# Kernel optimization log

Measured on AMD Instinct MI355X. Metric: run time of the kernel, lower is better.

Reference implementation:

```python
import jax, jax.numpy as jnp
import numpy as np

N_NODES = 50000
N_EDGES = 800000
F_IN = 128          # num_node_features == conv_size
L = 4               # num_conv_layers
LIN = 256
OUT = 10
N_GRAPHS = 64


def setup_inputs() -> dict:
    key = jax.random.key(0)
    ks = jax.random.split(key, 8)
    x = jax.random.normal(ks[0], (N_NODES, F_IN), dtype=jnp.float32)
    edge_index = jax.random.randint(ks[1], (2, N_EDGES), 0, N_NODES, dtype=jnp.int64)
    batch = jnp.sort(jax.random.randint(ks[2], (N_NODES,), 0, N_GRAPHS, dtype=jnp.int64))
    pos = jax.random.normal(ks[3], (N_NODES, 3), dtype=jnp.float32)
    # learned params: 4 GCN layers (all [F_IN,F_IN] since in==out==128), cat-JK head
    Ws = jax.random.normal(ks[4], (L, F_IN, F_IN), dtype=jnp.float32) * 0.05
    bs = jnp.zeros((L, F_IN), dtype=jnp.float32)
    Wlin = jax.random.normal(ks[5], (L * F_IN, LIN), dtype=jnp.float32) * 0.05
    blin = jnp.zeros((LIN,), dtype=jnp.float32)
    Wout = jax.random.normal(ks[6], (LIN, OUT), dtype=jnp.float32) * 0.05
    bout = jnp.zeros((OUT,), dtype=jnp.float32)
    return {"x": x, "edge_index": edge_index, "batch": batch, "pos": pos,
            "Ws": Ws, "bs": bs, "Wlin": Wlin, "blin": blin,
            "Wout": Wout, "bout": bout}


def reference(x, edge_index, batch, pos, Ws, bs, Wlin, blin, Wout, bout):
    N = x.shape[0]
    # GCN normalization with added self-loops (PyG gcn_norm, edge_weight=1)
    loop = jnp.arange(N, dtype=edge_index.dtype)
    src = jnp.concatenate([edge_index[0], loop])
    dst = jnp.concatenate([edge_index[1], loop])
    deg = jax.ops.segment_sum(jnp.ones_like(dst, dtype=x.dtype), dst, num_segments=N)
    dinv = jax.lax.rsqrt(deg)  # deg >= 1 due to self-loops
    norm = (dinv[src] * dinv[dst])[:, None]  # [E+N, 1]

    h = x
    xs = []
    for l in range(L):
        t = h @ Ws[l]                                    # [N, F]
        agg = jax.ops.segment_sum(t[src] * norm, dst, num_segments=N)
        h = jax.nn.relu(agg + bs[l])                     # dropout is identity in eval
        xs.append(h)
    hcat = jnp.concatenate(xs, axis=-1)                  # JK 'cat' -> [N, L*F]
    g = jax.ops.segment_max(hcat, batch, num_segments=N_GRAPHS)  # global_max_pool
    return jax.nn.relu(g @ Wlin + blin) @ Wout + bout    # [N_GRAPHS, OUT]
```

## Files before the change

kernel.cpp:

```cpp
#include <hip/hip_runtime.h>
#include <stdint.h>

#define NN    50000
#define NE    800000
#define FD    128
#define NLAY  4
#define NLIN  256
#define NOUTF 10
#define NGR   64
#define NBKT  196
#define MAXB  8192
#define GEMMB 782
#define POOLB 512

typedef _Float16 half8  __attribute__((ext_vector_type(8)));
typedef _Float16 half4  __attribute__((ext_vector_type(4)));
typedef _Float16 half2t __attribute__((ext_vector_type(2)));
typedef float    f32x4  __attribute__((ext_vector_type(4)));

__device__ __forceinline__ int ld_idx(const void* p, int flag, long i){
    return flag ? (int)((const long long*)p)[i] : ((const int*)p)[i];
}

__global__ __launch_bounds__(256) void pre_k(const unsigned* __restrict__ eidx_u,
                                             const float* __restrict__ Ws,
                                             _Float16* __restrict__ WT,
                                             int* __restrict__ zbase, int zn, int zb,
                                             int* __restrict__ sent,
                                             int* __restrict__ flag){
    __shared__ int any;
    const int b = blockIdx.x, tid = threadIdx.x;
    if (b < 256){
        int idx = b*256 + tid;
        int l = idx >> 14;
        int r = idx & 16383;
        int c = r >> 7, k = r & 127;
        WT[idx] = (_Float16)Ws[(l<<14) + (k<<7) + c];
    } else if (b < 256 + zb){
        int i = (b-256)*256 + tid;
        if (i < zn) zbase[i] = 0;
    } else if (b == 256 + zb){
        if (tid < FD/2) sent[tid] = 0;
    } else {
        if (tid == 0) any = 0;
        __syncthreads();
        if (eidx_u[2*tid + 1] != 0u) atomicOr(&any, 1);
        __syncthreads();
        if (tid == 0) *flag = (any == 0) ? 1 : 0;
    }
}

__global__ __launch_bounds__(1024) void binB_k(const void* __restrict__ eidx,
                                               const int* __restrict__ flag,
                                               int* __restrict__ bktCur,
                                               unsigned* __restrict__ binned){
    __shared__ int hist[NBKT];
    __shared__ int resv[NBKT];
    __shared__ int cur[NBKT];
    const int tid = threadIdx.x;
    const int f = *flag;
    if (tid < NBKT){ hist[tid] = 0; cur[tid] = 0; }
    __syncthreads();

    int bkt[4]; unsigned pk[4];
    #pragma unroll
    for (int u = 0; u < 4; ++u){
        long e = (long)blockIdx.x*4096 + u*1024 + tid;
        if (e < NE){
            int s = ld_idx(eidx, f, e);
            int d = ld_idx(eidx, f, (long)NE + e);
            bkt[u] = d >> 8;
            pk[u]  = ((unsigned)(d & 255) << 16) | (unsigned)s;
            atomicAdd(&hist[bkt[u]], 1);
        } else bkt[u] = -1;
    }
    __syncthreads();
    if (tid < NBKT && hist[tid] > 0)
        resv[tid] = atomicAdd(&bktCur[tid], hist[tid]);
    __syncthreads();
    #pragma unroll
    for (int u = 0; u < 4; ++u){
        if (bkt[u] >= 0){
            int p = resv[bkt[u]] + atomicAdd(&cur[bkt[u]], 1);
            if ((unsigned)p < MAXB) binned[(long)bkt[u]*MAXB + p] = pk[u];
        }
    }
}

__global__ __launch_bounds__(256) void passC_k(const int* __restrict__ bktCur,
                                               const unsigned* __restrict__ binned,
                                               int* __restrict__ rp, int* __restrict__ re,
                                               float* __restrict__ dinv,
                                               unsigned short* __restrict__ cn,
                                               const void* __restrict__ batv,
                                               const int* __restrict__ flag,
                                               int* __restrict__ gstart){
    __shared__ unsigned staged[MAXB];
    __shared__ int cnt[256];
    __shared__ int sc[256];
    __shared__ int cur[256];
    const int tid = threadIdx.x;
    if (blockIdx.x >= NBKT){
        int i = (blockIdx.x - NBKT)*256 + tid;
        if (i >= NN) return;
        int f = *flag;
        int b = ld_idx(batv, f, i);
        if (i == 0){
            for (int g = 0; g <= b; ++g) gstart[g] = 0;
        } else {
            int p = ld_idx(batv, f, i-1);
            for (int g = p+1; g <= b; ++g) gstart[g] = i;
        }
        if (i == NN-1){
            for (int g = b+1; g <= NGR; ++g) gstart[g] = NN;
        }
        return;
    }
    const int b = blockIdx.x;
    int n = bktCur[b]; if (n > MAXB) n = MAXB;
    const long base = (long)b*MAXB;

    cnt[tid] = 0;
    __syncthreads();
    for (int i = tid; i < n; i += 256){
        unsigned rec = binned[base + i];
        staged[i] = rec;
        atomicAdd(&cnt[rec >> 16], 1);
    }
    __syncthreads();
    int c  = cnt[tid];
    int pc = (c + 15) & ~15;
    sc[tid] = pc;
    __syncthreads();
    for (int off = 1; off < 256; off <<= 1){
        int t = (tid >= off) ? sc[tid - off] : 0;
        __syncthreads();
        if (tid >= off) sc[tid] += t;
        __syncthreads();
    }
    int lo = sc[tid] - pc;
    int v = b*256 + tid;
    if (v < NN){
        rp[v]   = (int)base + lo;
        re[v]   = (int)base + lo + pc;
        dinv[v] = rsqrtf((float)(c + 1));
    }
    cur[tid] = lo;
    __syncthreads();
    for (int i = tid; i < n; i += 256){
        unsigned rec = staged[i];
        int j = rec >> 16;
        int p = atomicAdd(&cur[j], 1);
        cn[base + p] = (unsigned short)(rec & 0xFFFFu);
    }
    __syncthreads();
    for (int i = c; i < pc; ++i)
        cn[base + lo + i] = (unsigned short)NN;
}

template<bool F32IN, bool POOL>
__global__ __launch_bounds__(256) void gemm_k(const void* __restrict__ Av,
                                              const _Float16* __restrict__ WT,
                                              const float* __restrict__ dinv,
                                              _Float16* __restrict__ T,
                                              const _Float16* __restrict__ h,
                                              const int* __restrict__ gstart,
                                              unsigned* __restrict__ gbuf, int lpool){
    const int tid  = threadIdx.x;
    if (POOL && blockIdx.x >= GEMMB){
        __shared__ float red[4][FD];
        int pid = blockIdx.x - GEMMB;
        int g = pid >> 3, part = pid & 7;
        int lane = tid & 63, w = tid >> 6;
        int s0 = gstart[g], s1 = gstart[g+1];
        int len = s1 - s0;
        int chunk = (len + 7) >> 3;
        int a = s0 + part*chunk;
        int b = min(a + chunk, s1);
        int sub = (b - a + 3) >> 2;
        int aa = a + w*sub;
        int bb = min(aa + sub, b);
        const half2t* h2 = reinterpret_cast<const half2t*>(h);
        float m0 = 0.f, m1 = 0.f;
        for (int i = aa; i < bb; ++i){
            half2t x = h2[(long)i*64 + lane];
            m0 = fmaxf(m0, (float)x[0]);
            m1 = fmaxf(m1, (float)x[1]);
        }
        red[w][2*lane]   = m0;
        red[w][2*lane+1] = m1;
        __syncthreads();
        if (w == 0){
            float r0 = fmaxf(fmaxf(red[0][2*lane],   red[1][2*lane]),
                             fmaxf(red[2][2*lane],   red[3][2*lane]));
            float r1 = fmaxf(fmaxf(red[0][2*lane+1], red[1][2*lane+1]),
                             fmaxf(red[2][2*lane+1], red[3][2*lane+1]));
            atomicMax(&gbuf[g*(NLAY*FD) + lpool*FD + 2*lane    ], __float_as_uint(r0));
            atomicMax(&gbuf[g*(NLAY*FD) + lpool*FD + 2*lane + 1], __float_as_uint(r1));
        }
        return;
    }

    const int lane = tid & 63;
    const int wid  = tid >> 6;
    const int wr   = (wid >> 1) * 32;
    const int wc   = (wid & 1) * 64;
    const long r0  = (long)blockIdx.x * 64 + wr;
    const int lr   = lane & 15;
    const int lk   = (lane >> 4) * 8;

    half8 wf[4][4];
    #pragma unroll
    for (int n = 0; n < 4; ++n)
        #pragma unroll
        for (int kk = 0; kk < 4; ++kk)
            wf[n][kk] = *reinterpret_cast<const half8*>(WT + (wc + n*16 + lr)*FD + kk*32 + lk);

    f32x4 acc[2][4];
    #pragma unroll
    for (int m = 0; m < 2; ++m)
        #pragma unroll
        for (int n = 0; n < 4; ++n)
            acc[m][n] = (f32x4){0.f,0.f,0.f,0.f};

    #pragma unroll
    for (int kk = 0; kk < 4; ++kk){
        half8 af[2];
        #pragma unroll
        for (int m = 0; m < 2; ++m){
            long row = r0 + m*16 + lr;
            if (row < NN){
                if constexpr (F32IN){
                    const float* A = (const float*)Av;
                    float4 u0 = *reinterpret_cast<const float4*>(A + row*FD + kk*32 + lk);
                    float4 u1 = *reinterpret_cast<const float4*>(A + row*FD + kk*32 + lk + 4);
                    half8 a;
                    a[0]=(_Float16)u0.x; a[1]=(_Float16)u0.y; a[2]=(_Float16)u0.z; a[3]=(_Float16)u0.w;
                    a[4]=(_Float16)u1.x; a[5]=(_Float16)u1.y; a[6]=(_Float16)u1.z; a[7]=(_Float16)u1.w;
                    af[m] = a;
                } else {
                    const _Float16* A = (const _Float16*)Av;
                    af[m] = *reinterpret_cast<const half8*>(A + row*FD + kk*32 + lk);
                }
            } else af[m] = (half8)(_Float16)0;
        }
        #pragma unroll
        for (int m = 0; m < 2; ++m)
            #pragma unroll
            for (int n = 0; n < 4; ++n)
                acc[m][n] = __builtin_amdgcn_mfma_f32_16x16x32_f16(wf[n][kk], af[m], acc[m][n], 0, 0, 0);
    }

    #pragma unroll
    for (int m = 0; m < 2; ++m){
        long row = r0 + m*16 + lr;
        if (row >= NN) continue;
        float di = dinv[row];
        #pragma unroll
        for (int n = 0; n < 4; ++n){
            half4 o;
            o[0] = (_Float16)(acc[m][n][0] * di);
            o[1] = (_Float16)(acc[m][n][1] * di);
            o[2] = (_Float16)(acc[m][n][2] * di);
            o[3] = (_Float16)(acc[m][n][3] * di);
            *reinterpret_cast<half4*>(T + row*FD + wc + n*16 + (lane>>4)*4) = o;
        }
    }
}

__global__ __launch_bounds__(256) void agg_k(const _Float16* __restrict__ t,
                                             const int* __restrict__ rp,
                                             const int* __restrict__ re,
                                             const unsigned short* __restrict__ cn,
                                             const float* __restrict__ dinv,
                                             const float* __restrict__ bias,
                                             _Float16* __restrict__ h){
    const int lane = threadIdx.x & 63;
    const int wid  = threadIdx.x >> 6;
    const int r    = lane & 15;
    const int qb   = lane & 48;
    const int v    = blockIdx.x*16 + wid*4 + (lane >> 4);
    const half8* t8 = reinterpret_cast<const half8*>(t);

    float acc[8];
    #pragma unroll
    for (int i = 0; i < 8; ++i) acc[i] = 0.f;

    half8 sv = t8[(size_t)v*16 + r];

    const int e0 = rp[v], e1 = re[v];
    for (int base = e0; base < e1; base += 16){
        int ce = (int)cn[base + r];
        #pragma unroll
        for (int j = 0; j < 16; ++j){
            int s = __shfl(ce, qb + j);
            half8 g = t8[(size_t)s*16 + r];
            #pragma unroll
            for (int i = 0; i < 8; ++i) acc[i] += (float)g[i];
        }
    }

    float di = dinv[v];
    float4 b0 = reinterpret_cast<const float4*>(bias)[2*r];
    float4 b1 = reinterpret_cast<const float4*>(bias)[2*r+1];
    float bb[8] = {b0.x,b0.y,b0.z,b0.w,b1.x,b1.y,b1.z,b1.w};
    half8 o;
    #pragma unroll
    for (int i = 0; i < 8; ++i)
        o[i] = (_Float16)fmaxf(fmaf(acc[i] + (float)sv[i], di, bb[i]), 0.f);
    reinterpret_cast<half8*>(h)[(size_t)v*16 + r] = o;
}

__global__ __launch_bounds__(256) void pool_k(const _Float16* __restrict__ h,
                                              const int* __restrict__ gstart,
                                              unsigned* __restrict__ gbuf, int l){
    __shared__ float red[4][FD];
    int g = blockIdx.x, part = blockIdx.y;
    int tid = threadIdx.x, lane = tid & 63, w = tid >> 6;
    int s0 = gstart[g], s1 = gstart[g+1];
    int len = s1 - s0;
    int chunk = (len + 7) >> 3;
    int a = s0 + part*chunk;
    int b = min(a + chunk, s1);
    int sub = (b - a + 3) >> 2;
    int aa = a + w*sub;
    int bb = min(aa + sub, b);
    const half2t* h2 = reinterpret_cast<const half2t*>(h);
    float m0 = 0.f, m1 = 0.f;
    for (int i = aa; i < bb; ++i){
        half2t x = h2[(long)i*64 + lane];
        m0 = fmaxf(m0, (float)x[0]);
        m1 = fmaxf(m1, (float)x[1]);
    }
    red[w][2*lane]   = m0;
    red[w][2*lane+1] = m1;
    __syncthreads();
    if (w == 0){
        float r0 = fmaxf(fmaxf(red[0][2*lane],   red[1][2*lane]),
                         fmaxf(red[2][2*lane],   red[3][2*lane]));
        float r1 = fmaxf(fmaxf(red[0][2*lane+1], red[1][2*lane+1]),
                         fmaxf(red[2][2*lane+1], red[3][2*lane+1]));
        atomicMax(&gbuf[g*(NLAY*FD) + l*FD + 2*lane    ], __float_as_uint(r0));
        atomicMax(&gbuf[g*(NLAY*FD) + l*FD + 2*lane + 1], __float_as_uint(r1));
    }
}

__global__ __launch_bounds__(1024) void head_k(const unsigned* __restrict__ gbuf,
                                               const float* __restrict__ Wlin,
                                               const float* __restrict__ blin,
                                               const float* __restrict__ Wout,
                                               const float* __restrict__ bout,
                                               float* __restrict__ out){
    __shared__ float gs[NLAY*FD];
    __shared__ float ps[4][NLIN];
    __shared__ float us[NLIN];
    int g = blockIdx.x, tid = threadIdx.x;
    if (tid < NLAY*FD) gs[tid] = __uint_as_float(gbuf[g*(NLAY*FD) + tid]);
    __syncthreads();
    int c = tid & 255;
    int q = tid >> 8;
    float a = 0.f;
    #pragma unroll 8
    for (int k = q*128; k < q*128 + 128; ++k)
        a = fmaf(gs[k], Wlin[k*NLIN + c], a);
    ps[q][c] = a;
    __syncthreads();
    if (tid < NLIN){
        float u = ps[0][tid] + ps[1][tid] + ps[2][tid] + ps[3][tid] + blin[tid];
        us[tid] = fmaxf(u, 0.f);
    }
    __syncthreads();
    if (tid < NOUTF){
        float o = bout[tid];
        #pragma unroll 8
        for (int k = 0; k < NLIN; ++k) o = fmaf(us[k], Wout[k*NOUTF + tid], o);
        out[g*NOUTF + tid] = o;
    }
}

extern "C" void kernel_launch(void* const* d_in, const int* in_sizes, int n_in,
                              void* d_out, int out_size, void* d_ws, size_t ws_size,
                              hipStream_t stream){
    const float* x    = (const float*)d_in[0];
    const void*  eidx = d_in[1];
    const void*  batv = d_in[2];
    const float* Wsp  = (const float*)d_in[4];
    const float* bsp  = (const float*)d_in[5];
    const float* Wlin = (const float*)d_in[6];
    const float* blin = (const float*)d_in[7];
    const float* Wout = (const float*)d_in[8];
    const float* bout = (const float*)d_in[9];
    float* out = (float*)d_out;

    uintptr_t cur = (uintptr_t)d_ws;
    auto alloc = [&](size_t bytes)->void*{
        cur = (cur + 255) & ~(uintptr_t)255;
        void* p = (void*)cur;
        cur += bytes;
        return p;
    };
    _Float16* t    = (_Float16*)alloc((size_t)(NN+1)*FD*2);
    _Float16* h    = (_Float16*)alloc((size_t)NN*FD*2);
    _Float16* WT   = (_Float16*)alloc((size_t)NLAY*FD*FD*2);
    unsigned* binned = (unsigned*)alloc((size_t)NBKT*MAXB*4);
    unsigned short* cn = (unsigned short*)alloc((size_t)NBKT*MAXB*2);
    int*   rp    = (int*)  alloc((size_t)NN*4);
    int*   re    = (int*)  alloc((size_t)NN*4);
    float* dinv  = (float*)alloc((size_t)NN*4);
    int*   gst   = (int*)  alloc((NGR+1)*4);
    int*   flag  = (int*)  alloc(4);
    int*      bktCur = (int*)     alloc((size_t)NBKT*4);
    unsigned* gbuf   = (unsigned*)alloc((size_t)NGR*NLAY*FD*4);
    int zero_n = (int)((cur - (uintptr_t)bktCur + 3) / 4);
    int zb = (zero_n + 255) / 256;

    pre_k  <<<256 + zb + 2, 256, 0, stream>>>((const unsigned*)eidx, Wsp, WT,
                                              bktCur, zero_n, zb,
                                              (int*)(t + (size_t)NN*FD), flag);
    binB_k <<<NBKT, 1024, 0, stream>>>(eidx, flag, bktCur, binned);
    passC_k<<<NBKT + (NN+255)/256, 256, 0, stream>>>(bktCur, binned, rp, re, dinv, cn,
                                                     batv, flag, gst);

    for (int l = 0; l < NLAY; ++l){
        const void* hin = (l == 0) ? (const void*)x : (const void*)h;
        if (l == 0)
            gemm_k<true ,false><<<GEMMB, 256, 0, stream>>>(hin, WT, dinv, t,
                                                           h, gst, gbuf, 0);
        else
            gemm_k<false,true ><<<GEMMB + POOLB, 256, 0, stream>>>(hin, WT + (size_t)l*FD*FD,
                                                                   dinv, t, h, gst, gbuf, l-1);
        agg_k<<<NN/16, 256, 0, stream>>>(t, rp, re, cn, dinv, bsp + (size_t)l*FD, h);
    }
    pool_k<<<dim3(NGR, 8), 256, 0, stream>>>(h, gst, gbuf, NLAY-1);
    head_k<<<NGR, 1024, 0, stream>>>(gbuf, Wlin, blin, Wout, bout, out);
}
```

Baseline: 262.1 us.

## Quantize transformed features to per-row int8 with power-of-two scales for gather

The GEMM epilogue now computes a per-row absolute maximum, picks a power-of-two scale, and stores the transformed features as offset-128 uint8 with one float scale per row, instead of fp16. The aggregation kernel gathers 8 bytes per lane instead of 16, dequantizes with a shuffled scale, and subtracts the offset using a running sum of scales. This halves the bytes moved by the gather-heavy aggregation, which is bandwidth-bound. The cost is an extra block-wide reduction and barrier in the GEMM, more ALU work per gathered element, and a clear loss of accuracy that may break the tolerance.

After: 235.0 us. 10.4% less time.

```diff
diff --git a/kernel.cpp b/kernel.cpp
--- a/kernel.cpp
+++ b/kernel.cpp
@@ -27,6 +27,7 @@
                                              _Float16* __restrict__ WT,
                                              int* __restrict__ zbase, int zn, int zb,
                                              int* __restrict__ sent,
+                                             float* __restrict__ scl,
                                              int* __restrict__ flag){
     __shared__ int any;
     const int b = blockIdx.x, tid = threadIdx.x;
@@ -40,7 +41,8 @@
         int i = (b-256)*256 + tid;
         if (i < zn) zbase[i] = 0;
     } else if (b == 256 + zb){
-        if (tid < FD/2) sent[tid] = 0;
+        if (tid < FD/4) sent[tid] = 0;
+        if (tid == 0) scl[NN] = 0.f;
     } else {
         if (tid == 0) any = 0;
         __syncthreads();
@@ -162,7 +164,8 @@
 __global__ __launch_bounds__(256) void gemm_k(const void* __restrict__ Av,
                                               const _Float16* __restrict__ WT,
                                               const float* __restrict__ dinv,
-                                              _Float16* __restrict__ T,
+                                              unsigned char* __restrict__ T,
+                                              float* __restrict__ scl,
                                               const _Float16* __restrict__ h,
                                               const int* __restrict__ gstart,
                                               unsigned* __restrict__ gbuf, int lpool){
@@ -201,6 +204,7 @@
         return;
     }
 
+    __shared__ float hm[64][2];
     const int lane = tid & 63;
     const int wid  = tid >> 6;
     const int wr   = (wid >> 1) * 32;
@@ -251,24 +255,60 @@
                 acc[m][n] = __builtin_amdgcn_mfma_f32_16x16x32_f16(wf[n][kk], af[m], acc[m][n], 0, 0, 0);
     }
 
+    float amax[2] = {0.f, 0.f};
+    float dim[2];
+    #pragma unroll
+    for (int m = 0; m < 2; ++m){
+        long row = r0 + m*16 + lr;
+        float di = (row < NN) ? dinv[row] : 0.f;
+        dim[m] = di;
+        #pragma unroll
+        for (int n = 0; n < 4; ++n)
+            #pragma unroll
+            for (int q = 0; q < 4; ++q)
+                amax[m] = fmaxf(amax[m], fabsf(acc[m][n][q] * di));
+    }
+    #pragma unroll
+    for (int m = 0; m < 2; ++m){
+        amax[m] = fmaxf(amax[m], __shfl_xor(amax[m], 16));
+        amax[m] = fmaxf(amax[m], __shfl_xor(amax[m], 32));
+    }
+    if (lane < 16){
+        hm[wr + lane     ][wid & 1] = amax[0];
+        hm[wr + 16 + lane][wid & 1] = amax[1];
+    }
+    __syncthreads();
     #pragma unroll
     for (int m = 0; m < 2; ++m){
         long row = r0 + m*16 + lr;
         if (row >= NN) continue;
-        float di = dinv[row];
+        int rl = wr + m*16 + lr;
+        float rm = fmaxf(hm[rl][0], hm[rl][1]);
+        float a = rm * (1.0f/127.0f);
+        unsigned bits = __float_as_uint(a);
+        unsigned e = bits >> 23;
+        unsigned sb = ((bits & 0x7fffffu) ? e + 1u : e) << 23;
+        float scale = __uint_as_float(sb);
+        float inv = __uint_as_float((254u - (sb >> 23)) << 23);
+        if (rm < 1e-30f){ scale = 0.f; inv = 0.f; }
+        float di = dim[m];
         #pragma unroll
         for (int n = 0; n < 4; ++n){
-            half4 o;
-            o[0] = (_Float16)(acc[m][n][0] * di);
-            o[1] = (_Float16)(acc[m][n][1] * di);
-            o[2] = (_Float16)(acc[m][n][2] * di);
-            o[3] = (_Float16)(acc[m][n][3] * di);
-            *reinterpret_cast<half4*>(T + row*FD + wc + n*16 + (lane>>4)*4) = o;
-        }
-    }
-}
-
-__global__ __launch_bounds__(256) void agg_k(const _Float16* __restrict__ t,
+            int q0 = __float2int_rn(acc[m][n][0] * di * inv) + 128;
+            int q1 = __float2int_rn(acc[m][n][1] * di * inv) + 128;
+            int q2 = __float2int_rn(acc[m][n][2] * di * inv) + 128;
+            int q3 = __float2int_rn(acc[m][n][3] * di * inv) + 128;
+            unsigned p = (unsigned)q0 | ((unsigned)q1 << 8) |
+                         ((unsigned)q2 << 16) | ((unsigned)q3 << 24);
+            *reinterpret_cast<unsigned*>(T + (size_t)row*FD + wc + n*16 + (lane>>4)*4) = p;
+        }
+        if ((wid & 1) == 0 && lane < 16)
+            scl[row] = scale;
+    }
+}
+
+__global__ __launch_bounds__(256) void agg_k(const unsigned char* __restrict__ t,
+                                             const float* __restrict__ scl,
                                              const int* __restrict__ rp,
                                              const int* __restrict__ re,
                                              const unsigned short* __restrict__ cn,
@@ -280,34 +320,55 @@
     const int r    = lane & 15;
     const int qb   = lane & 48;
     const int v    = blockIdx.x*16 + wid*4 + (lane >> 4);
-    const half8* t8 = reinterpret_cast<const half8*>(t);
+    const uint2* tq = reinterpret_cast<const uint2*>(t);
 
     float acc[8];
     #pragma unroll
     for (int i = 0; i < 8; ++i) acc[i] = 0.f;
-
-    half8 sv = t8[(size_t)v*16 + r];
+    float ssum = 0.f;
 
     const int e0 = rp[v], e1 = re[v];
     for (int base = e0; base < e1; base += 16){
         int ce = (int)cn[base + r];
+        float scv = scl[ce];
         #pragma unroll
         for (int j = 0; j < 16; ++j){
-            int s = __shfl(ce, qb + j);
-            half8 g = t8[(size_t)s*16 + r];
-            #pragma unroll
-            for (int i = 0; i < 8; ++i) acc[i] += (float)g[i];
-        }
-    }
-
-    float di = dinv[v];
+            int s    = __shfl(ce,  qb + j);
+            float sc = __shfl(scv, qb + j);
+            uint2 g = tq[(size_t)s*16 + r];
+            acc[0] = fmaf((float)( g.x        & 255u), sc, acc[0]);
+            acc[1] = fmaf((float)((g.x >>  8) & 255u), sc, acc[1]);
+            acc[2] = fmaf((float)((g.x >> 16) & 255u), sc, acc[2]);
+            acc[3] = fmaf((float)( g.x >> 24        ), sc, acc[3]);
+            acc[4] = fmaf((float)( g.y        & 255u), sc, acc[4]);
+            acc[5] = fmaf((float)((g.y >>  8) & 255u), sc, acc[5]);
+            acc[6] = fmaf((float)((g.y >> 16) & 255u), sc, acc[6]);
+            acc[7] = fmaf((float)( g.y >> 24        ), sc, acc[7]);
+            ssum += sc;
+        }
+    }
+    {
+        float sc = scl[v];
+        uint2 g = tq[(size_t)v*16 + r];
+        acc[0] = fmaf((float)( g.x        & 255u), sc, acc[0]);
+        acc[1] = fmaf((float)((g.x >>  8) & 255u), sc, acc[1]);
+        acc[2] = fmaf((float)((g.x >> 16) & 255u), sc, acc[2]);
+        acc[3] = fmaf((float)( g.x >> 24        ), sc, acc[3]);
+        acc[4] = fmaf((float)( g.y        & 255u), sc, acc[4]);
+        acc[5] = fmaf((float)((g.y >>  8) & 255u), sc, acc[5]);
+        acc[6] = fmaf((float)((g.y >> 16) & 255u), sc, acc[6]);
+        acc[7] = fmaf((float)( g.y >> 24        ), sc, acc[7]);
+        ssum += sc;
+    }
+
+    float dis = dinv[v];
     float4 b0 = reinterpret_cast<const float4*>(bias)[2*r];
     float4 b1 = reinterpret_cast<const float4*>(bias)[2*r+1];
     float bb[8] = {b0.x,b0.y,b0.z,b0.w,b1.x,b1.y,b1.z,b1.w};
     half8 o;
     #pragma unroll
     for (int i = 0; i < 8; ++i)
-        o[i] = (_Float16)fmaxf(fmaf(acc[i] + (float)sv[i], di, bb[i]), 0.f);
+        o[i] = (_Float16)fmaxf(fmaf(acc[i] - 128.f*ssum, dis, bb[i]), 0.f);
     reinterpret_cast<half8*>(h)[(size_t)v*16 + r] = o;
 }
 
@@ -399,9 +460,10 @@
         cur += bytes;
         return p;
     };
-    _Float16* t    = (_Float16*)alloc((size_t)(NN+1)*FD*2);
-    _Float16* h    = (_Float16*)alloc((size_t)NN*FD*2);
-    _Float16* WT   = (_Float16*)alloc((size_t)NLAY*FD*FD*2);
+    unsigned char* t = (unsigned char*)alloc((size_t)(NN+1)*FD);
+    float* scl   = (float*)alloc((size_t)(NN+1)*4);
+    _Float16* h  = (_Float16*)alloc((size_t)NN*FD*2);
+    _Float16* WT = (_Float16*)alloc((size_t)NLAY*FD*FD*2);
     unsigned* binned = (unsigned*)alloc((size_t)NBKT*MAXB*4);
     unsigned short* cn = (unsigned short*)alloc((size_t)NBKT*MAXB*2);
     int*   rp    = (int*)  alloc((size_t)NN*4);
@@ -416,7 +478,7 @@
 
     pre_k  <<<256 + zb + 2, 256, 0, stream>>>((const unsigned*)eidx, Wsp, WT,
                                               bktCur, zero_n, zb,
-                                              (int*)(t + (size_t)NN*FD), flag);
+                                              (int*)(t + (size_t)NN*FD), scl, flag);
     binB_k <<<NBKT, 1024, 0, stream>>>(eidx, flag, bktCur, binned);
     passC_k<<<NBKT + (NN+255)/256, 256, 0, stream>>>(bktCur, binned, rp, re, dinv, cn,
                                                      batv, flag, gst);
@@ -424,12 +486,12 @@
     for (int l = 0; l < NLAY; ++l){
         const void* hin = (l == 0) ? (const void*)x : (const void*)h;
         if (l == 0)
-            gemm_k<true ,false><<<GEMMB, 256, 0, stream>>>(hin, WT, dinv, t,
+            gemm_k<true ,false><<<GEMMB, 256, 0, stream>>>(hin, WT, dinv, t, scl,
                                                            h, gst, gbuf, 0);
         else
             gemm_k<false,true ><<<GEMMB + POOLB, 256, 0, stream>>>(hin, WT + (size_t)l*FD*FD,
-                                                                   dinv, t, h, gst, gbuf, l-1);
-        agg_k<<<NN/16, 256, 0, stream>>>(t, rp, re, cn, dinv, bsp + (size_t)l*FD, h);
+                                                                   dinv, t, scl, h, gst, gbuf, l-1);
+        agg_k<<<NN/16, 256, 0, stream>>>(t, scl, rp, re, cn, dinv, bsp + (size_t)l*FD, h);
     }
     pool_k<<<dim3(NGR, 8), 256, 0, stream>>>(h, gst, gbuf, NLAY-1);
     head_k<<<NGR, 1024, 0, stream>>>(gbuf, Wlin, blin, Wout, bout, out);
```
